# Performance work log

Measured on AMD Instinct MI355X. Metric: run time of the kernel, lower is better.

The kernel has to match this reference:

```python
import math
import jax, jax.numpy as jnp
import numpy as np

EMB = 1024
HEADS = 16
HEAD_DIM = EMB // HEADS
FF = 4 * EMB
EPS = 1e-5


def gelu_tanh(x):
    c = math.sqrt(2.0 / math.pi)
    return 0.5 * x * (1.0 + jnp.tanh(c * (x + 0.044715 * x ** 3)))


def layernorm(x, scale, shift):
    mean = jnp.mean(x, axis=-1, keepdims=True)
    var = jnp.var(x, axis=-1, keepdims=True)
    return scale * (x - mean) / jnp.sqrt(var + EPS) + shift


def setup_inputs() -> dict:
    key = jax.random.key(0)
    ks = jax.random.split(key, 10)
    s = 0.02
    return {
        "x": jax.random.normal(ks[0], (2, 2048, EMB), dtype=jnp.float32),
        "Wq": jax.random.normal(ks[1], (EMB, EMB), dtype=jnp.float32) * s,
        "Wk": jax.random.normal(ks[2], (EMB, EMB), dtype=jnp.float32) * s,
        "Wv": jax.random.normal(ks[3], (EMB, EMB), dtype=jnp.float32) * s,
        "Wo": jax.random.normal(ks[4], (EMB, EMB), dtype=jnp.float32) * s,
        "bo": jnp.zeros((EMB,), dtype=jnp.float32),
        "W1": jax.random.normal(ks[5], (EMB, FF), dtype=jnp.float32) * s,
        "b1": jnp.zeros((FF,), dtype=jnp.float32),
        "W2": jax.random.normal(ks[6], (FF, EMB), dtype=jnp.float32) * s,
        "b2": jnp.zeros((EMB,), dtype=jnp.float32),
        "ln1_scale": jnp.ones((EMB,), dtype=jnp.float32),
        "ln1_shift": jnp.zeros((EMB,), dtype=jnp.float32),
        "ln2_scale": jnp.ones((EMB,), dtype=jnp.float32),
        "ln2_shift": jnp.zeros((EMB,), dtype=jnp.float32),
    }


def reference(x, Wq, Wk, Wv, Wo, bo, W1, b1, W2, b2,
              ln1_scale, ln1_shift, ln2_scale, ln2_shift):
    B, S, D = x.shape
    # --- pre-LN causal MHA ---
    h = layernorm(x, ln1_scale, ln1_shift)
    q = (h @ Wq).reshape(B, S, HEADS, HEAD_DIM).transpose(0, 2, 1, 3)  # [B,H,S,d]
    k = (h @ Wk).reshape(B, S, HEADS, HEAD_DIM).transpose(0, 2, 1, 3)
    v = (h @ Wv).reshape(B, S, HEADS, HEAD_DIM).transpose(0, 2, 1, 3)
    scores = jnp.einsum("bhqd,bhkd->bhqk", q, k)  # [B,H,S,S]
    causal = jnp.triu(jnp.ones((S, S), dtype=bool), k=1)
    scores = jnp.where(causal, -jnp.inf, scores)
    attn = jax.nn.softmax(scores / math.sqrt(HEAD_DIM), axis=-1)
    ctx = jnp.einsum("bhqk,bhkd->bhqd", attn, v)  # [B,H,S,d]
    ctx = ctx.transpose(0, 2, 1, 3).reshape(B, S, D)
    x = x + (ctx @ Wo + bo)
    # --- FFN ---
    h = layernorm(x, ln2_scale, ln2_shift)
    h = gelu_tanh(h @ W1 + b1) @ W2 + b2
    return x + h
```

## Files before the change

kernel.cpp:

```cpp
#include <hip/hip_runtime.h>
#include <hip/hip_bf16.h>
#include <math.h>

#define EMB 1024
#define HEADS 16
#define HEAD_DIM 64
#define FF_DIM 4096
#define SEQ 2048
#define BATCH 2
#define NTOK (BATCH * SEQ)
#define LN_EPS 1e-5f
#define QKV_N 3072
#define Q_PRESCALE 0.18033688011112042f

typedef __attribute__((ext_vector_type(8))) short s8v;
typedef __attribute__((ext_vector_type(4))) float f4v;

__device__ __forceinline__ unsigned short f2bf(float f) {
    union { __hip_bfloat16 h; unsigned short u; } cv;
    cv.h = __float2bfloat16(f);
    return cv.u;
}

__device__ __forceinline__ float fast_exp2(float x) {
#if __has_builtin(__builtin_amdgcn_exp2f)
    return __builtin_amdgcn_exp2f(x);
#else
    return exp2f(x);
#endif
}

__device__ __forceinline__ float gelu_f(float x) {
    const float c = 0.7978845608028654f;
    float x3 = x * x * x;
    return 0.5f * x * (1.0f + tanhf(c * (x + 0.044715f * x3)));
}

#define GLDS(gp, lp)                                                        \
    __builtin_amdgcn_global_load_lds(                                       \
        (const __attribute__((address_space(1))) void*)(gp),                \
        (__attribute__((address_space(3))) void*)(lp), 16, 0, 0)

__global__ __launch_bounds__(256) void ln_bf16_kernel(const float* __restrict__ x,
                                                      const float* __restrict__ scale,
                                                      const float* __restrict__ shift,
                                                      unsigned short* __restrict__ out) {
    int row = blockIdx.x;
    int tid = threadIdx.x;
    const float4 xv = ((const float4*)(x + (size_t)row * EMB))[tid];
    float s  = xv.x + xv.y + xv.z + xv.w;
    float ss = xv.x * xv.x + xv.y * xv.y + xv.z * xv.z + xv.w * xv.w;
    __shared__ float2 red[256];
    red[tid] = make_float2(s, ss);
    __syncthreads();
    for (int off = 128; off > 0; off >>= 1) {
        if (tid < off) {
            red[tid].x += red[tid + off].x;
            red[tid].y += red[tid + off].y;
        }
        __syncthreads();
    }
    float mean = red[0].x * (1.0f / EMB);
    float var  = red[0].y * (1.0f / EMB) - mean * mean;
    float rstd = rsqrtf(var + LN_EPS);
    float4 sc4 = ((const float4*)scale)[tid];
    float4 sh4 = ((const float4*)shift)[tid];
    ushort4 o;
    o.x = f2bf(sc4.x * (xv.x - mean) * rstd + sh4.x);
    o.y = f2bf(sc4.y * (xv.y - mean) * rstd + sh4.y);
    o.z = f2bf(sc4.z * (xv.z - mean) * rstd + sh4.z);
    o.w = f2bf(sc4.w * (xv.w - mean) * rstd + sh4.w);
    *(ushort4*)(out + (size_t)row * EMB + tid * 4) = o;
}

__device__ __forceinline__ void tconv_tile(const float* __restrict__ W,
                                           unsigned short* __restrict__ Wt,
                                           int K, int N, int bx, int by, int tid) {
    __shared__ float t[64][65];
    int n0 = bx * 64, k0 = by * 64;
#pragma unroll
    for (int it = 0; it < 4; ++it) {
        int f = tid + it * 256;
        int r = f >> 4, c = (f & 15) * 4;
        float4 w = *(const float4*)(W + (size_t)(k0 + r) * N + n0 + c);
        t[r][c] = w.x; t[r][c + 1] = w.y; t[r][c + 2] = w.z; t[r][c + 3] = w.w;
    }
    __syncthreads();
#pragma unroll
    for (int it = 0; it < 4; ++it) {
        int f = tid + it * 256;
        int rn = f >> 4, ck = (f & 15) * 4;
        ushort4 o;
        o.x = f2bf(t[ck + 0][rn]);
        o.y = f2bf(t[ck + 1][rn]);
        o.z = f2bf(t[ck + 2][rn]);
        o.w = f2bf(t[ck + 3][rn]);
        *(ushort4*)(Wt + (size_t)(n0 + rn) * K + k0 + ck) = o;
    }
}

__global__ __launch_bounds__(256) void tconv_all_kernel(
    const float* __restrict__ Wq, const float* __restrict__ Wk,
    const float* __restrict__ Wv, const float* __restrict__ Wo,
    const float* __restrict__ W1, const float* __restrict__ W2,
    unsigned short* __restrict__ Wqkv_t, unsigned short* __restrict__ Wo_t,
    unsigned short* __restrict__ W1_t, unsigned short* __restrict__ W2_t) {
    int b = blockIdx.x;
    int tid = threadIdx.x;
    if (b < 256)        tconv_tile(Wq, Wqkv_t,                      EMB, EMB,    b & 15, b >> 4, tid);
    else if (b < 512)   tconv_tile(Wk, Wqkv_t + (size_t)1024 * EMB, EMB, EMB,    (b - 256) & 15, (b - 256) >> 4, tid);
    else if (b < 768)   tconv_tile(Wv, Wqkv_t + (size_t)2048 * EMB, EMB, EMB,    (b - 512) & 15, (b - 512) >> 4, tid);
    else if (b < 1024)  tconv_tile(Wo, Wo_t,                        EMB, EMB,    (b - 768) & 15, (b - 768) >> 4, tid);
    else if (b < 2048)  tconv_tile(W1, W1_t,                        EMB, FF_DIM, (b - 1024) & 63, (b - 1024) >> 6, tid);
    else                tconv_tile(W2, W2_t,                        FF_DIM, EMB, (b - 2048) & 15, (b - 2048) >> 4, tid);
}

__global__ __launch_bounds__(256) void reduce_kernel(const float* __restrict__ p0,
                                                     const float* __restrict__ p1,
                                                     const float* __restrict__ bias,
                                                     const float* __restrict__ residual,
                                                     float* __restrict__ out) {
    size_t i4 = ((size_t)blockIdx.x * 256 + threadIdx.x) * 4;
    float4 a = *(const float4*)(p0 + i4);
    float4 b = *(const float4*)(p1 + i4);
    float4 r = *(const float4*)(residual + i4);
    int col = (int)(i4 & (EMB - 1));
    float4 bs = *(const float4*)(bias + col);
    float4 o;
    o.x = a.x + b.x + r.x + bs.x;
    o.y = a.y + b.y + r.y + bs.y;
    o.z = a.z + b.z + r.z + bs.z;
    o.w = a.w + b.w + r.w + bs.w;
    *(float4*)(out + i4) = o;
}

__global__ __launch_bounds__(256) void reduce_ln_kernel(const float* __restrict__ p0,
                                                        const float* __restrict__ p1,
                                                        const float* __restrict__ bias,
                                                        const float* __restrict__ residual,
                                                        float* __restrict__ x1,
                                                        const float* __restrict__ scale,
                                                        const float* __restrict__ shift,
                                                        unsigned short* __restrict__ out) {
    int row = blockIdx.x;
    int tid = threadIdx.x;
    size_t i4 = (size_t)row * EMB + tid * 4;
    float4 a = *(const float4*)(p0 + i4);
    float4 b = *(const float4*)(p1 + i4);
    float4 r = *(const float4*)(residual + i4);
    float4 bs = *(const float4*)(bias + tid * 4);
    float4 xv;
    xv.x = a.x + b.x + r.x + bs.x;
    xv.y = a.y + b.y + r.y + bs.y;
    xv.z = a.z + b.z + r.z + bs.z;
    xv.w = a.w + b.w + r.w + bs.w;
    *(float4*)(x1 + i4) = xv;

    float s  = xv.x + xv.y + xv.z + xv.w;
    float ss = xv.x * xv.x + xv.y * xv.y + xv.z * xv.z + xv.w * xv.w;
    __shared__ float2 red[256];
    red[tid] = make_float2(s, ss);
    __syncthreads();
    for (int off = 128; off > 0; off >>= 1) {
        if (tid < off) {
            red[tid].x += red[tid + off].x;
            red[tid].y += red[tid + off].y;
        }
        __syncthreads();
    }
    float mean = red[0].x * (1.0f / EMB);
    float var  = red[0].y * (1.0f / EMB) - mean * mean;
    float rstd = rsqrtf(var + LN_EPS);
    float4 sc4 = ((const float4*)scale)[tid];
    float4 sh4 = ((const float4*)shift)[tid];
    ushort4 o;
    o.x = f2bf(sc4.x * (xv.x - mean) * rstd + sh4.x);
    o.y = f2bf(sc4.y * (xv.y - mean) * rstd + sh4.y);
    o.z = f2bf(sc4.z * (xv.z - mean) * rstd + sh4.z);
    o.w = f2bf(sc4.w * (xv.w - mean) * rstd + sh4.w);
    *(ushort4*)(out + i4) = o;
}

__global__ __launch_bounds__(256, 2) void gemm_wide_kernel(
    const unsigned short* __restrict__ A,
    const unsigned short* __restrict__ Bt,
    unsigned short* __restrict__ Cb,
    int M, int N, int K,
    const float* __restrict__ bias,
    int do_gelu, int qkv_mode,
    unsigned short* __restrict__ vt)
{
    __shared__ short As[2][4096];
    __shared__ short Bs[2][8192];

    int tid = threadIdx.x;
    int m0 = blockIdx.y * 128;
    int n0 = blockIdx.x * 256;
    int wv = tid >> 6, lane = tid & 63;
    int wr = wv >> 1, wc = wv & 1;
    int quad = lane >> 4, ln = lane & 15;

    f4v acc[4][8];
#pragma unroll
    for (int i = 0; i < 4; ++i)
#pragma unroll
        for (int j = 0; j < 8; ++j) {
            f4v z = {0.f, 0.f, 0.f, 0.f};
            acc[i][j] = z;
        }

    size_t Kby = (size_t)K << 1;
    const char* Ag0 = (const char*)A + (size_t)(m0 + (tid & 127)) * Kby + (tid >> 7) * 16;
    const char* Bg0 = (const char*)Bt + (size_t)(n0 + tid) * Kby;

    int nIter = K >> 5;
    GLDS(Ag0, (char*)As[0] + tid * 16);
    GLDS(Ag0 + 32, (char*)As[0] + tid * 16 + 4096);
#pragma unroll
    for (int i = 0; i < 4; ++i)
        GLDS(Bg0 + i * 16, (char*)Bs[0] + tid * 16 + i * 4096);

    for (int it = 0; it < nIter; ++it) {
        __syncthreads();
        if (it + 1 < nIter) {
            int kb = (it + 1) << 6;
            char* Ad = (char*)As[(it + 1) & 1] + tid * 16;
            char* Bd = (char*)Bs[(it + 1) & 1] + tid * 16;
            GLDS(Ag0 + kb, Ad);
            GLDS(Ag0 + kb + 32, Ad + 4096);
#pragma unroll
            for (int i = 0; i < 4; ++i)
                GLDS(Bg0 + kb + i * 16, Bd + i * 4096);
        }
        const short* Ab = As[it & 1];
        const short* Bb = Bs[it & 1];
        s8v af[4], bfr[8];
#pragma unroll
        for (int i = 0; i < 4; ++i)
            af[i] = *(const s8v*)(Ab + ((size_t)quad * 128 + wr * 64 + i * 16 + ln) * 8);
#pragma unroll
        for (int j = 0; j < 8; ++j)
            bfr[j] = *(const s8v*)(Bb + ((size_t)quad * 256 + wc * 128 + j * 16 + ln) * 8);
#pragma unroll
        for (int i = 0; i < 4; ++i)
#pragma unroll
            for (int j = 0; j < 8; ++j)
                acc[i][j] = __builtin_amdgcn_mfma_f32_16x16x32_bf16(af[i], bfr[j], acc[i][j], 0, 0, 0);
    }

    int cn  = n0 + wc * 128 + ln;
    int cm0 = m0 + wr * 64 + quad * 4;

    if (qkv_mode) {
        if (n0 < 2048) {
            float sc = (n0 < 1024) ? Q_PRESCALE : 1.0f;
#pragma unroll
            for (int j = 0; j < 8; ++j) {
                int gn = cn + j * 16;
#pragma unroll
                for (int i = 0; i < 4; ++i)
#pragma unroll
                    for (int r = 0; r < 4; ++r)
                        Cb[(size_t)(cm0 + i * 16 + r) * 2048 + gn] = f2bf(acc[i][j][r] * sc);
            }
        } else {
#pragma unroll
            for (int j = 0; j < 8; ++j) {
                int gn = cn + j * 16 - 2048;
#pragma unroll
                for (int i = 0; i < 4; ++i) {
                    int gm0 = cm0 + i * 16;
                    int bb = gm0 >> 11, s0 = gm0 & 2047;
                    ushort4 pk;
                    pk.x = f2bf(acc[i][j][0]);
                    pk.y = f2bf(acc[i][j][1]);
                    pk.z = f2bf(acc[i][j][2]);
                    pk.w = f2bf(acc[i][j][3]);
                    *(ushort4*)(vt + ((size_t)bb * 1024 + gn) * SEQ + s0) = pk;
                }
            }
        }
        return;
    }

#pragma unroll
    for (int j = 0; j < 8; ++j) {
        int gn = cn + j * 16;
        float bj = bias ? bias[gn] : 0.f;
#pragma unroll
        for (int i = 0; i < 4; ++i) {
#pragma unroll
            for (int r = 0; r < 4; ++r) {
                float vv = acc[i][j][r] + bj;
                if (do_gelu) vv = gelu_f(vv);
                Cb[(size_t)(cm0 + i * 16 + r) * N + gn] = f2bf(vv);
            }
        }
    }
}

__global__ __launch_bounds__(256) void gemm_bf16_kernel(
    const unsigned short* __restrict__ A,
    const unsigned short* __restrict__ Bt,
    float* __restrict__ Cf0,
    float* __restrict__ Cf1,
    int M, int N, int K, int Klen)
{
    __shared__ short As[2][4096];
    __shared__ short Bs[2][4096];

    int tid = threadIdx.x;
    int m0 = blockIdx.y * 128;
    int n0 = blockIdx.x * 128;
    int k0 = blockIdx.z * Klen;
    float* Cf = blockIdx.z ? Cf1 : Cf0;
    int wv = tid >> 6, lane = tid & 63;
    int wr = wv >> 1, wc = wv & 1;
    int quad = lane >> 4, ln = lane & 15;

    f4v acc[4][4];
#pragma unroll
    for (int i = 0; i < 4; ++i)
#pragma unroll
        for (int j = 0; j < 4; ++j) {
            f4v z = {0.f, 0.f, 0.f, 0.f};
            acc[i][j] = z;
        }

    int r0 = tid & 127;
    size_t Kby = (size_t)K << 1;
    const char* Ag0 = (const char*)A + (size_t)(m0 + r0) * Kby + (size_t)k0 * 2 + (tid >> 7) * 16;
    const char* Bg0 = (const char*)Bt + (size_t)(n0 + r0) * Kby + (size_t)k0 * 2 + (tid >> 7) * 16;

    int nIter = Klen >> 5;
    GLDS(Ag0, (char*)As[0] + tid * 16);
    GLDS(Ag0 + 32, (char*)As[0] + tid * 16 + 4096);
    GLDS(Bg0, (char*)Bs[0] + tid * 16);
    GLDS(Bg0 + 32, (char*)Bs[0] + tid * 16 + 4096);

    for (int it = 0; it < nIter; ++it) {
        __syncthreads();
        if (it + 1 < nIter) {
            int kb = (it + 1) << 6;
            char* Ad = (char*)As[(it + 1) & 1] + tid * 16;
            char* Bd = (char*)Bs[(it + 1) & 1] + tid * 16;
            GLDS(Ag0 + kb, Ad);
            GLDS(Ag0 + kb + 32, Ad + 4096);
            GLDS(Bg0 + kb, Bd);
            GLDS(Bg0 + kb + 32, Bd + 4096);
        }
        const short* Ab = As[it & 1];
        const short* Bb = Bs[it & 1];
        s8v af[4], bfr[4];
#pragma unroll
        for (int i = 0; i < 4; ++i)
            af[i] = *(const s8v*)(Ab + ((size_t)quad * 128 + wr * 64 + i * 16 + ln) * 8);
#pragma unroll
        for (int j = 0; j < 4; ++j)
            bfr[j] = *(const s8v*)(Bb + ((size_t)quad * 128 + wc * 64 + j * 16 + ln) * 8);
#pragma unroll
        for (int i = 0; i < 4; ++i)
#pragma unroll
            for (int j = 0; j < 4; ++j)
                acc[i][j] = __builtin_amdgcn_mfma_f32_16x16x32_bf16(af[i], bfr[j], acc[i][j], 0, 0, 0);
    }

    int cn  = n0 + wc * 64 + ln;
    int cm0 = m0 + wr * 64 + quad * 4;
#pragma unroll
    for (int j = 0; j < 4; ++j) {
        int gn = cn + j * 16;
#pragma unroll
        for (int i = 0; i < 4; ++i)
#pragma unroll
            for (int r = 0; r < 4; ++r)
                Cf[(size_t)(cm0 + i * 16 + r) * N + gn] = acc[i][j][r];
    }
}

__global__ __launch_bounds__(256) void flash_attn_mfma_kernel(
    const unsigned short* __restrict__ qk,
    const unsigned short* __restrict__ vt,
    unsigned short* __restrict__ ctx)
{
    int h  = blockIdx.x;
    int qt = (int)gridDim.y - 1 - (int)blockIdx.y;
    int b  = blockIdx.z;
    int tid = threadIdx.x;
    int w = tid >> 6, lane = tid & 63;
    int quad = lane >> 4, ln = lane & 15;

    __shared__ short Kb2[2][4096];
    __shared__ short Vb2[2][4096];
    __shared__ short Ps[4][32 * 72];

    size_t qrow0 = (size_t)b * SEQ + (size_t)qt * 128;
    int wrow0 = w * 32;

    s8v qf[2][2];
#pragma unroll
    for (int mb = 0; mb < 2; ++mb)
#pragma unroll
        for (int ks = 0; ks < 2; ++ks)
            qf[mb][ks] = *(const s8v*)(qk + (qrow0 + wrow0 + mb * 16 + ln) * 2048
                                          + h * 64 + ks * 32 + quad * 8);

    float l_part[2][4];
    f4v o[2][4];
#pragma unroll
    for (int mb = 0; mb < 2; ++mb) {
#pragma unroll
        for (int r = 0; r < 4; ++r) l_part[mb][r] = 0.f;
#pragma unroll
        for (int db = 0; db < 4; ++db) {
            f4v z = {0.f, 0.f, 0.f, 0.f};
            o[mb][db] = z;
        }
    }

    const unsigned short* kb_p = qk + (size_t)b * SEQ * 2048 + 1024 + h * 64;
    const unsigned short* vb_p = vt + ((size_t)b * 1024 + h * 64) * SEQ;
    short* Pw = Ps[w];

    int rr = tid & 63;
    const unsigned short* Kg0 = kb_p + (size_t)rr * 2048 + (tid >> 6) * 8;
    const unsigned short* Vg0 = vb_p + (size_t)rr * 2048 + (tid >> 6) * 8;

    int ktn = 2 * qt + 2;
    int ktmax_w = (qt * 128 + wrow0 + 31) >> 6;

    GLDS(Kg0, (char*)Kb2[0] + tid * 16);
    GLDS(Kg0 + 32, (char*)Kb2[0] + tid * 16 + 4096);
    GLDS(Vg0, (char*)Vb2[0] + tid * 16);
    GLDS(Vg0 + 32, (char*)Vb2[0] + tid * 16 + 4096);

    for (int kt = 0; kt < ktn; ++kt) {
        __syncthreads();
        if (kt + 1 < ktn) {
            int nb_ = (kt + 1) & 1;
            const unsigned short* ks_ = Kg0 + (size_t)(kt + 1) * 64 * 2048;
            const unsigned short* vs_ = Vg0 + (kt + 1) * 64;
            GLDS(ks_, (char*)Kb2[nb_] + tid * 16);
            GLDS(ks_ + 32, (char*)Kb2[nb_] + tid * 16 + 4096);
            GLDS(vs_, (char*)Vb2[nb_] + tid * 16);
            GLDS(vs_ + 32, (char*)Vb2[nb_] + tid * 16 + 4096);
        }
        if (kt > ktmax_w) continue;

        const short* Kl = Kb2[kt & 1];
        const short* Vl = Vb2[kt & 1];

        f4v s[2][4];
#pragma unroll
        for (int mb = 0; mb < 2; ++mb)
#pragma unroll
            for (int nb = 0; nb < 4; ++nb) {
                f4v z = {0.f, 0.f, 0.f, 0.f};
                s[mb][nb] = z;
            }
#pragma unroll
        for (int ks = 0; ks < 2; ++ks)
#pragma unroll
            for (int nb = 0; nb < 4; ++nb) {
                s8v kfr = *(const s8v*)(Kl + ((size_t)(ks * 4 + quad) * 64 + nb * 16 + ln) * 8);
#pragma unroll
                for (int mb = 0; mb < 2; ++mb)
                    s[mb][nb] = __builtin_amdgcn_mfma_f32_16x16x32_bf16(qf[mb][ks], kfr, s[mb][nb], 0, 0, 0);
            }

#pragma unroll
        for (int mb = 0; mb < 2; ++mb) {
#pragma unroll
            for (int r = 0; r < 4; ++r) {
                int rloc = mb * 16 + quad * 4 + r;
                int grow = qt * 128 + wrow0 + rloc;
                float p[4];
#pragma unroll
                for (int nb = 0; nb < 4; ++nb) {
                    int key = kt * 64 + nb * 16 + ln;
                    float e = fast_exp2(s[mb][nb][r]);
                    p[nb] = (key > grow) ? 0.f : e;
                }
                l_part[mb][r] += (p[0] + p[1]) + (p[2] + p[3]);
#pragma unroll
                for (int nb = 0; nb < 4; ++nb)
                    Pw[rloc * 72 + nb * 16 + ln] = f2bf(p[nb]);
            }
        }

#pragma unroll
        for (int ks = 0; ks < 2; ++ks) {
            s8v pf[2];
#pragma unroll
            for (int mb = 0; mb < 2; ++mb)
                pf[mb] = *(const s8v*)(Pw + (mb * 16 + ln) * 72 + ks * 32 + quad * 8);
#pragma unroll
            for (int db = 0; db < 4; ++db) {
                s8v vfr = *(const s8v*)(Vl + ((size_t)(ks * 4 + quad) * 64 + db * 16 + ln) * 8);
#pragma unroll
                for (int mb = 0; mb < 2; ++mb)
                    o[mb][db] = __builtin_amdgcn_mfma_f32_16x16x32_bf16(pf[mb], vfr, o[mb][db], 0, 0, 0);
            }
        }
    }

#pragma unroll
    for (int mb = 0; mb < 2; ++mb)
#pragma unroll
        for (int r = 0; r < 4; ++r) {
            float l = l_part[mb][r];
#pragma unroll
            for (int msk = 1; msk < 16; msk <<= 1)
                l += __shfl_xor(l, msk);
            float inv = 1.0f / l;
            size_t row = qrow0 + wrow0 + mb * 16 + quad * 4 + r;
#pragma unroll
            for (int db = 0; db < 4; ++db)
                ctx[row * EMB + h * 64 + db * 16 + ln] = f2bf(o[mb][db][r] * inv);
        }
}

extern "C" void kernel_launch(void* const* d_in, const int* in_sizes, int n_in,
                              void* d_out, int out_size, void* d_ws, size_t ws_size,
                              hipStream_t stream) {
    const float* x    = (const float*)d_in[0];
    const float* Wq   = (const float*)d_in[1];
    const float* Wk   = (const float*)d_in[2];
    const float* Wv   = (const float*)d_in[3];
    const float* Wo   = (const float*)d_in[4];
    const float* bo   = (const float*)d_in[5];
    const float* W1   = (const float*)d_in[6];
    const float* b1   = (const float*)d_in[7];
    const float* W2   = (const float*)d_in[8];
    const float* b2   = (const float*)d_in[9];
    const float* ln1s = (const float*)d_in[10];
    const float* ln1b = (const float*)d_in[11];
    const float* ln2s = (const float*)d_in[12];
    const float* ln2b = (const float*)d_in[13];
    float* out = (float*)d_out;

    const size_t MiB = 1024 * 1024;
    uint8_t* w8 = (uint8_t*)d_ws;
    unsigned short* Wqkv_t = (unsigned short*)(w8);
    unsigned short* Wo_t   = (unsigned short*)(w8 +  6 * MiB);
    unsigned short* W1_t   = (unsigned short*)(w8 +  8 * MiB);
    unsigned short* W2_t   = (unsigned short*)(w8 + 16 * MiB);
    unsigned short* act_bf = (unsigned short*)(w8 + 24 * MiB);
    unsigned short* qk_bf  = (unsigned short*)(w8 + 32 * MiB);
    unsigned short* vt     = (unsigned short*)(w8 + 48 * MiB);
    float*          p0a    = (float*)(w8 + 32 * MiB);
    float*          p1a    = (float*)(w8 + 48 * MiB);
    unsigned short* u_bf   = (unsigned short*)(w8 + 32 * MiB);
    float*          x1     = (float*)(w8 + 64 * MiB);
    float*          p0b    = (float*)(w8);
    float*          p1b    = (float*)(w8 + 80 * MiB);

    tconv_all_kernel<<<3072, 256, 0, stream>>>(Wq, Wk, Wv, Wo, W1, W2,
                                               Wqkv_t, Wo_t, W1_t, W2_t);

    ln_bf16_kernel<<<NTOK, 256, 0, stream>>>(x, ln1s, ln1b, act_bf);

    gemm_wide_kernel<<<dim3(QKV_N / 256, NTOK / 128), 256, 0, stream>>>(
        act_bf, Wqkv_t, qk_bf, NTOK, QKV_N, EMB, nullptr, 0, 1, vt);

    flash_attn_mfma_kernel<<<dim3(HEADS, SEQ / 128, BATCH), 256, 0, stream>>>(qk_bf, vt, act_bf);

    gemm_bf16_kernel<<<dim3(EMB / 128, NTOK / 128, 2), 256, 0, stream>>>(
        act_bf, Wo_t, p0a, p1a, NTOK, EMB, EMB, 512);
    reduce_ln_kernel<<<NTOK, 256, 0, stream>>>(p0a, p1a, bo, x, x1, ln2s, ln2b, act_bf);

    gemm_wide_kernel<<<dim3(FF_DIM / 256, NTOK / 128), 256, 0, stream>>>(
        act_bf, W1_t, u_bf, NTOK, FF_DIM, EMB, b1, 1, 0, nullptr);

    gemm_bf16_kernel<<<dim3(EMB / 128, NTOK / 128, 2), 256, 0, stream>>>(
        u_bf, W2_t, p0b, p1b, NTOK, EMB, FF_DIM, 2048);
    reduce_kernel<<<(NTOK * EMB) / 1024, 256, 0, stream>>>(p0b, p1b, b2, x1, out);
}
```

Baseline: 472.3 us.

## Replace wide GEMM with 256x256-tile 8-wave phased pipeline kernel

Replaces the 128x256-tile, 4-wave double-buffered GEMM used for the QKV and W1 projections with a 256x256-tile, 512-thread kernel. It uses a K-step of 128 and explicit barrier and waitcnt phases that interleave LDS reads, direct-to-LDS global loads and MFMA quarters at raised priority. It also adds an XCD-aware block-index swizzle over a 1D grid. The aim is better arithmetic intensity and overlap of memory traffic with MFMA work. In exchange it uses 128 KB of LDS and many barriers, which lowers occupancy and adds sync overhead.

```diff
diff --git a/kernel.cpp b/kernel.cpp
--- a/kernel.cpp
+++ b/kernel.cpp
@@ -40,6 +40,11 @@
     __builtin_amdgcn_global_load_lds(                                       \
         (const __attribute__((address_space(1))) void*)(gp),                \
         (__attribute__((address_space(3))) void*)(lp), 16, 0, 0)
+
+#define BAR()   do { __builtin_amdgcn_s_barrier(); __builtin_amdgcn_sched_barrier(0); } while (0)
+#define LGKM0() do { asm volatile("s_waitcnt lgkmcnt(0)" ::: "memory"); __builtin_amdgcn_sched_barrier(0); } while (0)
+#define VMC4()  do { asm volatile("s_waitcnt vmcnt(4)" ::: "memory"); __builtin_amdgcn_sched_barrier(0); } while (0)
+#define VMC0()  do { asm volatile("s_waitcnt vmcnt(0)" ::: "memory"); __builtin_amdgcn_sched_barrier(0); } while (0)
 
 __global__ __launch_bounds__(256) void ln_bf16_kernel(const float* __restrict__ x,
                                                       const float* __restrict__ scale,
@@ -181,7 +186,7 @@
     *(ushort4*)(out + i4) = o;
 }
 
-__global__ __launch_bounds__(256, 2) void gemm_wide_kernel(
+__global__ __launch_bounds__(512, 2) void gemm_8ph_kernel(
     const unsigned short* __restrict__ A,
     const unsigned short* __restrict__ Bt,
     unsigned short* __restrict__ Cb,
@@ -190,92 +195,150 @@
     int do_gelu, int qkv_mode,
     unsigned short* __restrict__ vt)
 {
-    __shared__ short As[2][4096];
-    __shared__ short Bs[2][8192];
+    __shared__ short lds[65536];
 
     int tid = threadIdx.x;
-    int m0 = blockIdx.y * 128;
-    int n0 = blockIdx.x * 256;
-    int wv = tid >> 6, lane = tid & 63;
-    int wr = wv >> 1, wc = wv & 1;
+    int w = tid >> 6, lane = tid & 63;
+    int wr = w >> 2, wc = w & 3;
     int quad = lane >> 4, ln = lane & 15;
 
-    f4v acc[4][8];
-#pragma unroll
-    for (int i = 0; i < 4; ++i)
-#pragma unroll
-        for (int j = 0; j < 8; ++j) {
-            f4v z = {0.f, 0.f, 0.f, 0.f};
-            acc[i][j] = z;
-        }
+    int nbx = N >> 8;
+    int nwg = (M >> 8) * nbx;
+    int bid = (int)blockIdx.x;
+    int swz = (nwg & 7) ? bid : ((bid & 7) * (nwg >> 3) + (bid >> 3));
+    int by = swz / nbx, bx = swz - by * nbx;
+    int m0 = by << 8, n0 = bx << 8;
+
+    f4v acc[8][4];
+#pragma unroll
+    for (int i = 0; i < 8; ++i)
+#pragma unroll
+        for (int j = 0; j < 4; ++j) { f4v z = {0.f, 0.f, 0.f, 0.f}; acc[i][j] = z; }
 
     size_t Kby = (size_t)K << 1;
-    const char* Ag0 = (const char*)A + (size_t)(m0 + (tid & 127)) * Kby + (tid >> 7) * 16;
-    const char* Bg0 = (const char*)Bt + (size_t)(n0 + tid) * Kby;
-
-    int nIter = K >> 5;
-    GLDS(Ag0, (char*)As[0] + tid * 16);
-    GLDS(Ag0 + 32, (char*)As[0] + tid * 16 + 4096);
-#pragma unroll
-    for (int i = 0; i < 4; ++i)
-        GLDS(Bg0 + i * 16, (char*)Bs[0] + tid * 16 + i * 4096);
-
+    size_t AhS = (size_t)128 * Kby;
+    const char* AgC = (const char*)A + (size_t)(m0 + (tid & 127)) * Kby + (size_t)((tid >> 7) << 4);
+    const char* BgC = (const char*)Bt + (size_t)(n0 + (tid & 127)) * Kby + (size_t)((tid >> 7) << 4);
+    char* ldsC = (char*)lds;
+    int tid16 = tid << 4;
+
+    const short* aRd = lds + wr * 8192 + quad * 1024 + ln * 8;
+    const short* bRd = lds + 32768 + (wc >> 1) * 8192 + (wc & 1) * 512 + quad * 1024 + ln * 8;
+
+#define STG_A(tb, h, b) do {                                                     \
+    const char* s_ = AgC + (size_t)(h) * AhS + (size_t)(tb);                     \
+    char* d_ = ldsC + (b) * 32768 + (h) * 16384 + tid16;                         \
+    GLDS(s_, d_); GLDS(s_ + 64, d_ + 8192); } while (0)
+#define STG_B(tb, h, b) do {                                                     \
+    const char* s_ = BgC + (size_t)(h) * AhS + (size_t)(tb);                     \
+    char* d_ = ldsC + 65536 + (b) * 32768 + (h) * 16384 + tid16;                 \
+    GLDS(s_, d_); GLDS(s_ + 64, d_ + 8192); } while (0)
+#define RD_A4(mg, b) do {                                                        \
+    _Pragma("unroll") for (int f_ = 0; f_ < 4; ++f_) {                           \
+        af[f_][0] = *(const s8v*)(aRd + (b) * 16384 + ((mg) * 4 + f_) * 128);    \
+        af[f_][1] = *(const s8v*)(aRd + (b) * 16384 + 4096 + ((mg) * 4 + f_) * 128); } } while (0)
+#define RD_B2(dst, ng, b) do {                                                   \
+    _Pragma("unroll") for (int g_ = 0; g_ < 2; ++g_) {                           \
+        dst[g_][0] = *(const s8v*)(bRd + (b) * 16384 + ((ng) * 2 + g_) * 128);   \
+        dst[g_][1] = *(const s8v*)(bRd + (b) * 16384 + 4096 + ((ng) * 2 + g_) * 128); } } while (0)
+#define MF_Q(mg, bsrc, ng) do {                                                  \
+    __builtin_amdgcn_s_setprio(1);                                               \
+    _Pragma("unroll") for (int f_ = 0; f_ < 4; ++f_)                             \
+    _Pragma("unroll") for (int g_ = 0; g_ < 2; ++g_)                             \
+    _Pragma("unroll") for (int k_ = 0; k_ < 2; ++k_)                             \
+        acc[(mg) * 4 + f_][(ng) * 2 + g_] = __builtin_amdgcn_mfma_f32_16x16x32_bf16( \
+            af[f_][k_], bsrc[g_][k_], acc[(mg) * 4 + f_][(ng) * 2 + g_], 0, 0, 0); \
+    __builtin_amdgcn_s_setprio(0); } while (0)
+
+    s8v af[4][2], bf0[2][2], bf1[2][2];
+
+    STG_A(0, 0, 0); STG_A(0, 1, 0);
+    STG_B(0, 0, 0); STG_B(0, 1, 0);
+    STG_B(128, 0, 1); STG_B(128, 1, 1);
+    VMC4();
+    BAR();
+
+    int nIter = K >> 7;
     for (int it = 0; it < nIter; ++it) {
-        __syncthreads();
-        if (it + 1 < nIter) {
-            int kb = (it + 1) << 6;
-            char* Ad = (char*)As[(it + 1) & 1] + tid * 16;
-            char* Bd = (char*)Bs[(it + 1) & 1] + tid * 16;
-            GLDS(Ag0 + kb, Ad);
-            GLDS(Ag0 + kb + 32, Ad + 4096);
-#pragma unroll
-            for (int i = 0; i < 4; ++i)
-                GLDS(Bg0 + kb + i * 16, Bd + i * 4096);
-        }
-        const short* Ab = As[it & 1];
-        const short* Bb = Bs[it & 1];
-        s8v af[4], bfr[8];
-#pragma unroll
-        for (int i = 0; i < 4; ++i)
-            af[i] = *(const s8v*)(Ab + ((size_t)quad * 128 + wr * 64 + i * 16 + ln) * 8);
-#pragma unroll
-        for (int j = 0; j < 8; ++j)
-            bfr[j] = *(const s8v*)(Bb + ((size_t)quad * 256 + wc * 128 + j * 16 + ln) * 8);
-#pragma unroll
-        for (int i = 0; i < 4; ++i)
-#pragma unroll
-            for (int j = 0; j < 8; ++j)
-                acc[i][j] = __builtin_amdgcn_mfma_f32_16x16x32_bf16(af[i], bfr[j], acc[i][j], 0, 0, 0);
-    }
-
-    int cn  = n0 + wc * 128 + ln;
-    int cm0 = m0 + wr * 64 + quad * 4;
+        size_t base = (size_t)it << 8;
+        bool pf = (it + 1 < nIter);
+
+        RD_A4(0, 0); RD_B2(bf0, 0, 0);
+        STG_A(base + 128, 0, 1);
+        BAR(); LGKM0();
+        MF_Q(0, bf0, 0);
+        BAR();
+        RD_B2(bf1, 1, 0);
+        STG_A(base + 128, 1, 1);
+        BAR(); LGKM0();
+        MF_Q(0, bf1, 1);
+        BAR();
+        RD_A4(1, 0);
+        if (pf) STG_B(base + 256, 0, 0);
+        BAR(); LGKM0();
+        MF_Q(1, bf0, 0);
+        BAR();
+        if (pf) STG_B(base + 256, 1, 0);
+        BAR();
+        MF_Q(1, bf1, 1);
+        if (pf) { VMC4(); } else { VMC0(); }
+        BAR();
+
+        RD_A4(0, 1); RD_B2(bf0, 0, 1);
+        if (pf) STG_A(base + 256, 0, 0);
+        BAR(); LGKM0();
+        MF_Q(0, bf0, 0);
+        BAR();
+        RD_B2(bf1, 1, 1);
+        if (pf) STG_A(base + 256, 1, 0);
+        BAR(); LGKM0();
+        MF_Q(0, bf1, 1);
+        BAR();
+        RD_A4(1, 1);
+        if (pf) STG_B(base + 384, 0, 1);
+        BAR(); LGKM0();
+        MF_Q(1, bf0, 0);
+        BAR();
+        if (pf) STG_B(base + 384, 1, 1);
+        BAR();
+        MF_Q(1, bf1, 1);
+        if (pf) VMC4();
+        BAR();
+    }
+#undef STG_A
+#undef STG_B
+#undef RD_A4
+#undef RD_B2
+#undef MF_Q
+
+    int cn  = n0 + wc * 64 + ln;
+    int cm0 = m0 + wr * 128 + quad * 4;
 
     if (qkv_mode) {
         if (n0 < 2048) {
             float sc = (n0 < 1024) ? Q_PRESCALE : 1.0f;
 #pragma unroll
-            for (int j = 0; j < 8; ++j) {
-                int gn = cn + j * 16;
-#pragma unroll
-                for (int i = 0; i < 4; ++i)
+            for (int g = 0; g < 4; ++g) {
+                int gn = cn + g * 16;
+#pragma unroll
+                for (int f = 0; f < 8; ++f)
 #pragma unroll
                     for (int r = 0; r < 4; ++r)
-                        Cb[(size_t)(cm0 + i * 16 + r) * 2048 + gn] = f2bf(acc[i][j][r] * sc);
+                        Cb[(size_t)(cm0 + f * 16 + r) * 2048 + gn] = f2bf(acc[f][g][r] * sc);
             }
         } else {
 #pragma unroll
-            for (int j = 0; j < 8; ++j) {
-                int gn = cn + j * 16 - 2048;
-#pragma unroll
-                for (int i = 0; i < 4; ++i) {
-                    int gm0 = cm0 + i * 16;
+            for (int g = 0; g < 4; ++g) {
+                int gn = cn + g * 16 - 2048;
+#pragma unroll
+                for (int f = 0; f < 8; ++f) {
+                    int gm0 = cm0 + f * 16;
                     int bb = gm0 >> 11, s0 = gm0 & 2047;
                     ushort4 pk;
-                    pk.x = f2bf(acc[i][j][0]);
-                    pk.y = f2bf(acc[i][j][1]);
-                    pk.z = f2bf(acc[i][j][2]);
-                    pk.w = f2bf(acc[i][j][3]);
+                    pk.x = f2bf(acc[f][g][0]);
+                    pk.y = f2bf(acc[f][g][1]);
+                    pk.z = f2bf(acc[f][g][2]);
+                    pk.w = f2bf(acc[f][g][3]);
                     *(ushort4*)(vt + ((size_t)bb * 1024 + gn) * SEQ + s0) = pk;
                 }
             }
@@ -284,18 +347,17 @@
     }
 
 #pragma unroll
-    for (int j = 0; j < 8; ++j) {
-        int gn = cn + j * 16;
+    for (int g = 0; g < 4; ++g) {
+        int gn = cn + g * 16;
         float bj = bias ? bias[gn] : 0.f;
 #pragma unroll
-        for (int i = 0; i < 4; ++i) {
+        for (int f = 0; f < 8; ++f)
 #pragma unroll
             for (int r = 0; r < 4; ++r) {
-                float vv = acc[i][j][r] + bj;
+                float vv = acc[f][g][r] + bj;
                 if (do_gelu) vv = gelu_f(vv);
-                Cb[(size_t)(cm0 + i * 16 + r) * N + gn] = f2bf(vv);
+                Cb[(size_t)(cm0 + f * 16 + r) * N + gn] = f2bf(vv);
             }
-        }
     }
 }
 
@@ -560,7 +622,7 @@
 
     ln_bf16_kernel<<<NTOK, 256, 0, stream>>>(x, ln1s, ln1b, act_bf);
 
-    gemm_wide_kernel<<<dim3(QKV_N / 256, NTOK / 128), 256, 0, stream>>>(
+    gemm_8ph_kernel<<<(NTOK / 256) * (QKV_N / 256), 512, 0, stream>>>(
         act_bf, Wqkv_t, qk_bf, NTOK, QKV_N, EMB, nullptr, 0, 1, vt);
 
     flash_attn_mfma_kernel<<<dim3(HEADS, SEQ / 128, BATCH), 256, 0, stream>>>(qk_bf, vt, act_bf);
@@ -569,7 +631,7 @@
         act_bf, Wo_t, p0a, p1a, NTOK, EMB, EMB, 512);
     reduce_ln_kernel<<<NTOK, 256, 0, stream>>>(p0a, p1a, bo, x, x1, ln2s, ln2b, act_bf);
 
-    gemm_wide_kernel<<<dim3(FF_DIM / 256, NTOK / 128), 256, 0, stream>>>(
+    gemm_8ph_kernel<<<(NTOK / 256) * (FF_DIM / 256), 512, 0, stream>>>(
         act_bf, W1_t, u_bf, NTOK, FF_DIM, EMB, b1, 1, 0, nullptr);
 
     gemm_bf16_kernel<<<dim3(EMB / 128, NTOK / 128, 2), 256, 0, stream>>>(
```

Measured after the change: 428.0 us. 1.1x faster.
